# Performance work log

Measured on AMD Instinct MI355X. Metric: run time of the kernel, lower is better.

The kernel has to match this reference:

```python
import jax, jax.numpy as jnp
from jax import lax
import numpy as np

H = 64  # LSTM_HIDDEN_DIM
I = 3   # NUM_WEATHER_FEATURES


def _lstm_layer(x_seq, w_ih, w_hh, b_ih, b_hh):
    # x_seq: [B, T, in]; w_ih: [4H, in]; w_hh: [4H, H]; b_*: [4H]
    B = x_seq.shape[0]
    # Precompute input projections for all timesteps: [T, B, 4H]
    gx = jnp.einsum('bti,gi->tbg', x_seq, w_ih) + (b_ih + b_hh)
    h0 = jnp.zeros((B, H), dtype=x_seq.dtype)
    c0 = jnp.zeros((B, H), dtype=x_seq.dtype)

    def step(carry, g_t):
        h, c = carry
        gates = g_t + h @ w_hh.T  # [B, 4H]
        i, f, g, o = jnp.split(gates, 4, axis=-1)  # PyTorch gate order i,f,g,o
        i = jax.nn.sigmoid(i)
        f = jax.nn.sigmoid(f)
        g = jnp.tanh(g)
        o = jax.nn.sigmoid(o)
        c = f * c + i * g
        h = o * jnp.tanh(c)
        return (h, c), h

    (h_T, _), hs = lax.scan(step, (h0, c0), gx)
    # hs: [T, B, H] -> [B, T, H]
    return jnp.transpose(hs, (1, 0, 2)), h_T


def setup_inputs() -> dict:
    key = jax.random.key(0)
    ks = jax.random.split(key, 9)
    s = 1.0 / np.sqrt(H)  # PyTorch LSTM init scale
    x = jax.random.normal(ks[0], (4096, 365, I), dtype=jnp.float32)
    return {
        'x': x,
        'w_ih0': jax.random.uniform(ks[1], (4 * H, I), jnp.float32, -s, s),
        'w_hh0': jax.random.uniform(ks[2], (4 * H, H), jnp.float32, -s, s),
        'b_ih0': jax.random.uniform(ks[3], (4 * H,), jnp.float32, -s, s),
        'b_hh0': jax.random.uniform(ks[4], (4 * H,), jnp.float32, -s, s),
        'w_ih1': jax.random.uniform(ks[5], (4 * H, H), jnp.float32, -s, s),
        'w_hh1': jax.random.uniform(ks[6], (4 * H, H), jnp.float32, -s, s),
        'b_ih1': jax.random.uniform(ks[7], (4 * H,), jnp.float32, -s, s),
        'b_hh1': jax.random.uniform(ks[8], (4 * H,), jnp.float32, -s, s),
    }


def reference(x, w_ih0, w_hh0, b_ih0, b_hh0, w_ih1, w_hh1, b_ih1, b_hh1):
    # Layer 1 over raw features
    h1_seq, _ = _lstm_layer(x, w_ih0, w_hh0, b_ih0, b_hh0)
    # Layer 2 over layer-1 hidden states (eval mode: inter-layer dropout disabled)
    _, h2_T = _lstm_layer(h1_seq, w_ih1, w_hh1, b_ih1, b_hh1)
    # forward returns h_n[-1] == final hidden state of top layer: [B, H]
    return h2_T
```

## Files before the change

### kernel.cpp

```cpp
#include <hip/hip_runtime.h>

#define TT 365
#define NB 16
#define NTH 1024
#define XLEN (NB * TT * 3)

typedef _Float16 halfx8 __attribute__((ext_vector_type(8)));
typedef float floatx4 __attribute__((ext_vector_type(4)));
typedef float floatx2 __attribute__((ext_vector_type(2)));

#define MMH(A, B, C) __builtin_amdgcn_mfma_f32_16x16x32_f16((A), (B), (C), 0, 0, 0)

#define SGP -2.8853900817779268f
#define SGN  2.8853900817779268f
#define SS_  -1.4426950408889634f

static __device__ __forceinline__ float rcpf(float x) { return __builtin_amdgcn_rcpf(x); }
static __device__ __forceinline__ float ex2(float x)  { return __builtin_amdgcn_exp2f(x); }
static __device__ __forceinline__ unsigned short h16(float v) {
  _Float16 h = (_Float16)v;
  return __builtin_bit_cast(unsigned short, h);
}

#define LOADFRAG(SRC, SCALE, HI)                                               \
  do {                                                                         \
    _Pragma("unroll")                                                          \
    for (int jj = 0; jj < 8; ++jj) {                                           \
      (HI)[jj] = (_Float16)((SCALE) * (SRC)[jj]);                              \
    }                                                                          \
  } while (0)

#define PTAIL_CORE(PA, PB, CS2, HOUT)                                          \
  const floatx2 one_ = {1.0f, 1.0f};                                           \
  const floatx2 ei_ = {ex2((PA)[0]), ex2((PB)[0])};                            \
  const floatx2 ef_ = {ex2((PA)[1]), ex2((PB)[1])};                            \
  const floatx2 eg_ = {ex2((PA)[2]), ex2((PB)[2])};                            \
  const floatx2 eo_ = {ex2((PA)[3]), ex2((PB)[3])};                            \
  const floatx2 fd_ = one_ + ef_;                                              \
  const floatx2 fr_ = {rcpf(fd_.x), rcpf(fd_.y)};                              \
  const floatx2 P1_ = (one_ + ei_) * (one_ + eg_);                             \
  const floatx2 R1_ = {rcpf(P1_.x), rcpf(P1_.y)};                              \
  const floatx2 sgn2_ = {SGN, SGN};                                            \
  const floatx2 sgp2_ = {SGP, SGP};                                            \
  (CS2) = fr_ * (CS2) + (sgn2_ * eg_ + sgp2_) * R1_;                           \
  (CS2).x = fminf((CS2).x, 126.0f);                                            \
  (CS2).y = fminf((CS2).y, 126.0f);                                            \
  const floatx2 ec_ = {ex2((CS2).x), ex2((CS2).y)};                            \
  const floatx2 P2_ = (one_ + eo_) * (one_ + ec_);                             \
  const floatx2 R2_ = {rcpf(P2_.x), rcpf(P2_.y)};                              \
  const floatx2 HOUT = (one_ - ec_) * R2_;

#define PTAIL(PA, PB, CS2, ZW, IA, IB)                                         \
  do {                                                                         \
    PTAIL_CORE(PA, PB, CS2, hv_)                                               \
    (ZW)[IA] = h16(hv_.x);                                                     \
    (ZW)[IB] = h16(hv_.y);                                                     \
  } while (0)

__global__ __launch_bounds__(NTH)
__attribute__((amdgpu_waves_per_eu(4, 4)))
void lstm2_mfma10(
    const float* __restrict__ x,
    const float* __restrict__ w_ih0, const float* __restrict__ w_hh0,
    const float* __restrict__ b_ih0, const float* __restrict__ b_hh0,
    const float* __restrict__ w_ih1, const float* __restrict__ w_hh1,
    const float* __restrict__ b_ih1, const float* __restrict__ b_hh1,
    float* __restrict__ out)
{
  __shared__ __align__(16) unsigned short Z[2][2048];
  __shared__ __align__(16) float xlds[XLEN];

  const int tid  = threadIdx.x;
  const int lane = tid & 63;
  const int wv   = tid >> 6;
  const int n15  = lane & 15;
  const int quad = lane >> 4;
  const int bbase = blockIdx.x * NB;
  const float sA = ((n15 & 3) == 2) ? SGP : SS_;

  {
    const float* xg = x + (size_t)bbase * (TT * 3);
    for (int i = tid; i < XLEN; i += NTH) xlds[i] = xg[i];
    for (int i = tid; i < 2048; i += NTH) { Z[0][i] = 0; Z[1][i] = 0; }
  }
  unsigned short* const Zb0 = &Z[0][0];
  unsigned short* const Zb1 = &Z[1][0];
  __syncthreads();

  if (wv < 8) {
    const int w = wv;
    halfx8 a2[2][4];
    floatx4 b1v[2];
    #pragma unroll
    for (int tt = 0; tt < 2; ++tt) {
      const int mt   = 2 * w + tt;
      const int arow = (n15 & 3) * 64 + mt * 4 + (n15 >> 2);
      #pragma unroll
      for (int kt = 0; kt < 4; ++kt) {
        const int k0 = kt * 32 + quad * 8;
        const float* src = (k0 < 64) ? (w_ih1 + arow * 64 + k0)
                                     : (w_hh1 + arow * 64 + (k0 - 64));
        LOADFRAG(src, sA, a2[tt][kt]);
      }
      #pragma unroll
      for (int r = 0; r < 4; ++r) {
        const int crow = r * 64 + mt * 4 + quad;
        const float sC = (r == 2) ? SGP : SS_;
        b1v[tt][r] = sC * (b_ih1[crow] + b_hh1[crow]);
      }
    }
    const int j0 = 8 * w + quad, j1 = 8 * w + 4 + quad;
    const int si0 = 1024 + (j0 >> 5) * 512 + ((j0 >> 3) & 3) * 128 + n15 * 8 + (j0 & 7);
    const int si1 = 1024 + (j1 >> 5) * 512 + ((j1 >> 3) & 3) * 128 + n15 * 8 + (j1 & 7);
    floatx2 c2v = {0.f, 0.f};
    const halfx8* const Z0r = (const halfx8*)Zb0 + lane;
    const halfx8* const Z1r = (const halfx8*)Zb1 + lane;

    __syncthreads();

#define ESTEP(ZRP, ZW)                                                         \
    do {                                                                       \
      const halfx8 bh0 = (ZRP)[0],   bh1 = (ZRP)[64];                          \
      const halfx8 bh2 = (ZRP)[128], bh3 = (ZRP)[192];                         \
      floatx4 e0 = b1v[0], e1 = b1v[1];                                        \
      e0 = MMH(a2[0][0], bh0, e0); e0 = MMH(a2[0][1], bh1, e0);                \
      e0 = MMH(a2[0][2], bh2, e0); e0 = MMH(a2[0][3], bh3, e0);                \
      e1 = MMH(a2[1][0], bh0, e1); e1 = MMH(a2[1][1], bh1, e1);                \
      e1 = MMH(a2[1][2], bh2, e1); e1 = MMH(a2[1][3], bh3, e1);                \
      PTAIL(e0, e1, c2v, ZW, si0, si1);                                        \
      __syncthreads();                                                         \
    } while (0)

    for (int it = 0; it < 182; ++it) {
      ESTEP(Z0r, Zb1);
      ESTEP(Z1r, Zb0);
    }

    {
      const halfx8 bh0 = Z0r[0],   bh1 = Z0r[64];
      const halfx8 bh2 = Z0r[128], bh3 = Z0r[192];
      floatx4 e0 = b1v[0], e1 = b1v[1];
      e0 = MMH(a2[0][0], bh0, e0); e0 = MMH(a2[0][1], bh1, e0);
      e0 = MMH(a2[0][2], bh2, e0); e0 = MMH(a2[0][3], bh3, e0);
      e1 = MMH(a2[1][0], bh0, e1); e1 = MMH(a2[1][1], bh1, e1);
      e1 = MMH(a2[1][2], bh2, e1); e1 = MMH(a2[1][3], bh3, e1);
      PTAIL_CORE(e0, e1, c2v, hv_)
      out[(size_t)(bbase + n15) * 64 + j0] = hv_.x;
      out[(size_t)(bbase + n15) * 64 + j1] = hv_.y;
    }
  } else {
    const int u = wv - 8;
    halfx8 a1[2][2];
    floatx4 wiX[2], wiY[2], wiZ[2], b0v[2];
    #pragma unroll
    for (int tt = 0; tt < 2; ++tt) {
      const int mt   = 2 * u + tt;
      const int arow = (n15 & 3) * 64 + mt * 4 + (n15 >> 2);
      #pragma unroll
      for (int kt = 0; kt < 2; ++kt) {
        const float* src = w_hh0 + arow * 64 + kt * 32 + quad * 8;
        LOADFRAG(src, sA, a1[tt][kt]);
      }
      #pragma unroll
      for (int r = 0; r < 4; ++r) {
        const int crow = r * 64 + mt * 4 + quad;
        const float sC = (r == 2) ? SGP : SS_;
        wiX[tt][r] = sC * w_ih0[crow * 3 + 0];
        wiY[tt][r] = sC * w_ih0[crow * 3 + 1];
        wiZ[tt][r] = sC * w_ih0[crow * 3 + 2];
        b0v[tt][r] = sC * (b_ih0[crow] + b_hh0[crow]);
      }
    }
    const int j0 = 8 * u + quad, j1 = 8 * u + 4 + quad;
    const int si0 = (j0 >> 5) * 512 + ((j0 >> 3) & 3) * 128 + n15 * 8 + (j0 & 7);
    const int si1 = (j1 >> 5) * 512 + ((j1 >> 3) & 3) * 128 + n15 * 8 + (j1 & 7);
    floatx2 c1v = {0.f, 0.f};
    const halfx8* const Z0r = (const halfx8*)Zb0 + lane;
    const halfx8* const Z1r = (const halfx8*)Zb1 + lane;

    {
      const float xv0 = xlds[n15 * 1095 + 0];
      const float xv1 = xlds[n15 * 1095 + 1];
      const float xv2 = xlds[n15 * 1095 + 2];
      const floatx4 s0 = {xv0, xv0, xv0, xv0};
      const floatx4 s1 = {xv1, xv1, xv1, xv1};
      const floatx4 s2 = {xv2, xv2, xv2, xv2};
      floatx4 d0 = __builtin_elementwise_fma(wiX[0], s0,
                     __builtin_elementwise_fma(wiY[0], s1,
                       __builtin_elementwise_fma(wiZ[0], s2, b0v[0])));
      floatx4 d1 = __builtin_elementwise_fma(wiX[1], s0,
                     __builtin_elementwise_fma(wiY[1], s1,
                       __builtin_elementwise_fma(wiZ[1], s2, b0v[1])));
      PTAIL(d0, d1, c1v, Zb0, si0, si1);
    }
    __syncthreads();

    const float* xp = xlds + n15 * 1095 + 3;

#define DSTEP(ZRP, ZW)                                                         \
    do {                                                                       \
      const halfx8 bh0 = (ZRP)[0], bh1 = (ZRP)[64];                            \
      const float xv0 = xp[0], xv1 = xp[1], xv2 = xp[2];                       \
      const floatx4 s0 = {xv0, xv0, xv0, xv0};                                 \
      const floatx4 s1 = {xv1, xv1, xv1, xv1};                                 \
      const floatx4 s2 = {xv2, xv2, xv2, xv2};                                 \
      floatx4 d0 = __builtin_elementwise_fma(wiX[0], s0,                       \
                     __builtin_elementwise_fma(wiY[0], s1,                     \
                       __builtin_elementwise_fma(wiZ[0], s2, b0v[0])));        \
      floatx4 d1 = __builtin_elementwise_fma(wiX[1], s0,                       \
                     __builtin_elementwise_fma(wiY[1], s1,                     \
                       __builtin_elementwise_fma(wiZ[1], s2, b0v[1])));        \
      d0 = MMH(a1[0][0], bh0, d0); d0 = MMH(a1[0][1], bh1, d0);                \
      d1 = MMH(a1[1][0], bh0, d1); d1 = MMH(a1[1][1], bh1, d1);                \
      PTAIL(d0, d1, c1v, ZW, si0, si1);                                        \
      xp += 3;                                                                 \
      __syncthreads();                                                         \
    } while (0)

    for (int it = 0; it < 182; ++it) {
      DSTEP(Z0r, Zb1);
      DSTEP(Z1r, Zb0);
    }
  }
}

extern "C" void kernel_launch(void* const* d_in, const int* in_sizes, int n_in,
                              void* d_out, int out_size, void* d_ws, size_t ws_size,
                              hipStream_t stream) {
  const float* x     = (const float*)d_in[0];
  const float* w_ih0 = (const float*)d_in[1];
  const float* w_hh0 = (const float*)d_in[2];
  const float* b_ih0 = (const float*)d_in[3];
  const float* b_hh0 = (const float*)d_in[4];
  const float* w_ih1 = (const float*)d_in[5];
  const float* w_hh1 = (const float*)d_in[6];
  const float* b_ih1 = (const float*)d_in[7];
  const float* b_hh1 = (const float*)d_in[8];
  float* out = (float*)d_out;

  const int B = in_sizes[0] / (TT * 3);
  const int grid = B / NB;

  lstm2_mfma10<<<dim3(grid), dim3(NTH), 0, stream>>>(
      x, w_ih0, w_hh0, b_ih0, b_hh0, w_ih1, w_hh1, b_ih1, b_hh1, out);
}
```

Measured before the change: 311.9 us.

## Pack hidden-state writes, transpose x in LDS, merge cell-update reciprocals

Gate rows are remapped so each lane owns two adjacent hidden units. Their fp16 outputs can then be packed with cvt_pkrtz into one 32-bit LDS store per step instead of two 16-bit stores, and the final output is written as a float2. The input sequence is transposed in LDS to a [t][batch][4] layout so each step reads x with one 16-byte load. The cell update folds its two reciprocals into one with a common denominator, and the clamp is lowered to 60 to keep the larger product from overflowing. This shortens the per-step serial dependency chain. It risks precision loss from the product denominator and adds integer divides in the prologue.

```diff
diff --git a/kernel.cpp b/kernel.cpp
--- a/kernel.cpp
+++ b/kernel.cpp
@@ -17,10 +17,6 @@
 
 static __device__ __forceinline__ float rcpf(float x) { return __builtin_amdgcn_rcpf(x); }
 static __device__ __forceinline__ float ex2(float x)  { return __builtin_amdgcn_exp2f(x); }
-static __device__ __forceinline__ unsigned short h16(float v) {
-  _Float16 h = (_Float16)v;
-  return __builtin_bit_cast(unsigned short, h);
-}
 
 #define LOADFRAG(SRC, SCALE, HI)                                               \
   do {                                                                         \
@@ -36,30 +32,31 @@
   const floatx2 ef_ = {ex2((PA)[1]), ex2((PB)[1])};                            \
   const floatx2 eg_ = {ex2((PA)[2]), ex2((PB)[2])};                            \
   const floatx2 eo_ = {ex2((PA)[3]), ex2((PB)[3])};                            \
-  const floatx2 fd_ = one_ + ef_;                                              \
-  const floatx2 fr_ = {rcpf(fd_.x), rcpf(fd_.y)};                              \
-  const floatx2 P1_ = (one_ + ei_) * (one_ + eg_);                             \
-  const floatx2 R1_ = {rcpf(P1_.x), rcpf(P1_.y)};                              \
   const floatx2 sgn2_ = {SGN, SGN};                                            \
   const floatx2 sgp2_ = {SGP, SGP};                                            \
-  (CS2) = fr_ * (CS2) + (sgn2_ * eg_ + sgp2_) * R1_;                           \
-  (CS2).x = fminf((CS2).x, 126.0f);                                            \
-  (CS2).y = fminf((CS2).y, 126.0f);                                            \
+  const floatx2 fd_ = one_ + ef_;                                              \
+  const floatx2 P1_ = (one_ + ei_) * (one_ + eg_);                             \
+  const floatx2 Dp_ = P1_ * fd_;                                               \
+  const floatx2 R_  = {rcpf(Dp_.x), rcpf(Dp_.y)};                              \
+  const floatx2 T_  = (sgn2_ * eg_ + sgp2_) * fd_;                             \
+  (CS2) = ((CS2) * P1_ + T_) * R_;                                             \
+  (CS2).x = fminf((CS2).x, 60.0f);                                             \
+  (CS2).y = fminf((CS2).y, 60.0f);                                             \
   const floatx2 ec_ = {ex2((CS2).x), ex2((CS2).y)};                            \
   const floatx2 P2_ = (one_ + eo_) * (one_ + ec_);                             \
   const floatx2 R2_ = {rcpf(P2_.x), rcpf(P2_.y)};                              \
   const floatx2 HOUT = (one_ - ec_) * R2_;
 
-#define PTAIL(PA, PB, CS2, ZW, IA, IB)                                         \
+#define PTAIL(PA, PB, CS2, ZW32, WIDX)                                         \
   do {                                                                         \
     PTAIL_CORE(PA, PB, CS2, hv_)                                               \
-    (ZW)[IA] = h16(hv_.x);                                                     \
-    (ZW)[IB] = h16(hv_.y);                                                     \
+    (ZW32)[WIDX] =                                                             \
+        __builtin_bit_cast(unsigned, __builtin_amdgcn_cvt_pkrtz(hv_.x, hv_.y)); \
   } while (0)
 
 __global__ __launch_bounds__(NTH)
 __attribute__((amdgpu_waves_per_eu(4, 4)))
-void lstm2_mfma10(
+void lstm2_mfma11(
     const float* __restrict__ x,
     const float* __restrict__ w_ih0, const float* __restrict__ w_hh0,
     const float* __restrict__ b_ih0, const float* __restrict__ b_hh0,
@@ -68,7 +65,7 @@
     float* __restrict__ out)
 {
   __shared__ __align__(16) unsigned short Z[2][2048];
-  __shared__ __align__(16) float xlds[XLEN];
+  __shared__ __align__(16) float xh[TT * 16 * 4];
 
   const int tid  = threadIdx.x;
   const int lane = tid & 63;
@@ -80,12 +77,19 @@
 
   {
     const float* xg = x + (size_t)bbase * (TT * 3);
-    for (int i = tid; i < XLEN; i += NTH) xlds[i] = xg[i];
+    for (int i = tid; i < XLEN; i += NTH) {
+      const int b = i / 1095;
+      const int rem = i - b * 1095;
+      const int t = rem / 3;
+      const int c = rem - 3 * t;
+      xh[(t * 16 + b) * 4 + c] = xg[i];
+    }
     for (int i = tid; i < 2048; i += NTH) { Z[0][i] = 0; Z[1][i] = 0; }
   }
   unsigned short* const Zb0 = &Z[0][0];
   unsigned short* const Zb1 = &Z[1][0];
   __syncthreads();
+
 
   if (wv < 8) {
     const int w = wv;
@@ -93,8 +97,7 @@
     floatx4 b1v[2];
     #pragma unroll
     for (int tt = 0; tt < 2; ++tt) {
-      const int mt   = 2 * w + tt;
-      const int arow = (n15 & 3) * 64 + mt * 4 + (n15 >> 2);
+      const int arow = (n15 & 3) * 64 + 8 * w + 2 * (n15 >> 2) + tt;
       #pragma unroll
       for (int kt = 0; kt < 4; ++kt) {
         const int k0 = kt * 32 + quad * 8;
@@ -104,21 +107,20 @@
       }
       #pragma unroll
       for (int r = 0; r < 4; ++r) {
-        const int crow = r * 64 + mt * 4 + quad;
+        const int crow = r * 64 + 8 * w + 2 * quad + tt;
         const float sC = (r == 2) ? SGP : SS_;
         b1v[tt][r] = sC * (b_ih1[crow] + b_hh1[crow]);
       }
     }
-    const int j0 = 8 * w + quad, j1 = 8 * w + 4 + quad;
-    const int si0 = 1024 + (j0 >> 5) * 512 + ((j0 >> 3) & 3) * 128 + n15 * 8 + (j0 & 7);
-    const int si1 = 1024 + (j1 >> 5) * 512 + ((j1 >> 3) & 3) * 128 + n15 * 8 + (j1 & 7);
+    const int j0 = 8 * w + 2 * quad;
+    const int widx = 512 + (w >> 2) * 256 + (w & 3) * 64 + n15 * 4 + quad;
     floatx2 c2v = {0.f, 0.f};
     const halfx8* const Z0r = (const halfx8*)Zb0 + lane;
     const halfx8* const Z1r = (const halfx8*)Zb1 + lane;
 
     __syncthreads();
 
-#define ESTEP(ZRP, ZW)                                                         \
+#define ESTEP(ZRP, ZW32)                                                       \
     do {                                                                       \
       const halfx8 bh0 = (ZRP)[0],   bh1 = (ZRP)[64];                          \
       const halfx8 bh2 = (ZRP)[128], bh3 = (ZRP)[192];                         \
@@ -127,13 +129,13 @@
       e0 = MMH(a2[0][2], bh2, e0); e0 = MMH(a2[0][3], bh3, e0);                \
       e1 = MMH(a2[1][0], bh0, e1); e1 = MMH(a2[1][1], bh1, e1);                \
       e1 = MMH(a2[1][2], bh2, e1); e1 = MMH(a2[1][3], bh3, e1);                \
-      PTAIL(e0, e1, c2v, ZW, si0, si1);                                        \
+      PTAIL(e0, e1, c2v, ZW32, widx);                                          \
       __syncthreads();                                                         \
     } while (0)
 
     for (int it = 0; it < 182; ++it) {
-      ESTEP(Z0r, Zb1);
-      ESTEP(Z1r, Zb0);
+      ESTEP(Z0r, (unsigned*)Zb1);
+      ESTEP(Z1r, (unsigned*)Zb0);
     }
 
     {
@@ -145,8 +147,7 @@
       e1 = MMH(a2[1][0], bh0, e1); e1 = MMH(a2[1][1], bh1, e1);
       e1 = MMH(a2[1][2], bh2, e1); e1 = MMH(a2[1][3], bh3, e1);
       PTAIL_CORE(e0, e1, c2v, hv_)
-      out[(size_t)(bbase + n15) * 64 + j0] = hv_.x;
-      out[(size_t)(bbase + n15) * 64 + j1] = hv_.y;
+      *(floatx2*)(out + (size_t)(bbase + n15) * 64 + j0) = hv_;
     }
   } else {
     const int u = wv - 8;
@@ -154,8 +155,7 @@
     floatx4 wiX[2], wiY[2], wiZ[2], b0v[2];
     #pragma unroll
     for (int tt = 0; tt < 2; ++tt) {
-      const int mt   = 2 * u + tt;
-      const int arow = (n15 & 3) * 64 + mt * 4 + (n15 >> 2);
+      const int arow = (n15 & 3) * 64 + 8 * u + 2 * (n15 >> 2) + tt;
       #pragma unroll
       for (int kt = 0; kt < 2; ++kt) {
         const float* src = w_hh0 + arow * 64 + kt * 32 + quad * 8;
@@ -163,7 +163,7 @@
       }
       #pragma unroll
       for (int r = 0; r < 4; ++r) {
-        const int crow = r * 64 + mt * 4 + quad;
+        const int crow = r * 64 + 8 * u + 2 * quad + tt;
         const float sC = (r == 2) ? SGP : SS_;
         wiX[tt][r] = sC * w_ih0[crow * 3 + 0];
         wiY[tt][r] = sC * w_ih0[crow * 3 + 1];
@@ -171,39 +171,35 @@
         b0v[tt][r] = sC * (b_ih0[crow] + b_hh0[crow]);
       }
     }
-    const int j0 = 8 * u + quad, j1 = 8 * u + 4 + quad;
-    const int si0 = (j0 >> 5) * 512 + ((j0 >> 3) & 3) * 128 + n15 * 8 + (j0 & 7);
-    const int si1 = (j1 >> 5) * 512 + ((j1 >> 3) & 3) * 128 + n15 * 8 + (j1 & 7);
+    const int widx = (u >> 2) * 256 + (u & 3) * 64 + n15 * 4 + quad;
     floatx2 c1v = {0.f, 0.f};
     const halfx8* const Z0r = (const halfx8*)Zb0 + lane;
     const halfx8* const Z1r = (const halfx8*)Zb1 + lane;
 
     {
-      const float xv0 = xlds[n15 * 1095 + 0];
-      const float xv1 = xlds[n15 * 1095 + 1];
-      const float xv2 = xlds[n15 * 1095 + 2];
-      const floatx4 s0 = {xv0, xv0, xv0, xv0};
-      const floatx4 s1 = {xv1, xv1, xv1, xv1};
-      const floatx4 s2 = {xv2, xv2, xv2, xv2};
+      const floatx4 xv = *(const floatx4*)(xh + n15 * 4);
+      const floatx4 s0 = {xv[0], xv[0], xv[0], xv[0]};
+      const floatx4 s1 = {xv[1], xv[1], xv[1], xv[1]};
+      const floatx4 s2 = {xv[2], xv[2], xv[2], xv[2]};
       floatx4 d0 = __builtin_elementwise_fma(wiX[0], s0,
                      __builtin_elementwise_fma(wiY[0], s1,
                        __builtin_elementwise_fma(wiZ[0], s2, b0v[0])));
       floatx4 d1 = __builtin_elementwise_fma(wiX[1], s0,
                      __builtin_elementwise_fma(wiY[1], s1,
                        __builtin_elementwise_fma(wiZ[1], s2, b0v[1])));
-      PTAIL(d0, d1, c1v, Zb0, si0, si1);
+      PTAIL(d0, d1, c1v, (unsigned*)Zb0, widx);
     }
     __syncthreads();
 
-    const float* xp = xlds + n15 * 1095 + 3;
-
-#define DSTEP(ZRP, ZW)                                                         \
+    const float* xp = xh + 64 + n15 * 4;
+
+#define DSTEP(ZRP, ZW32)                                                       \
     do {                                                                       \
       const halfx8 bh0 = (ZRP)[0], bh1 = (ZRP)[64];                            \
-      const float xv0 = xp[0], xv1 = xp[1], xv2 = xp[2];                       \
-      const floatx4 s0 = {xv0, xv0, xv0, xv0};                                 \
-      const floatx4 s1 = {xv1, xv1, xv1, xv1};                                 \
-      const floatx4 s2 = {xv2, xv2, xv2, xv2};                                 \
+      const floatx4 xv = *(const floatx4*)xp;                                  \
+      const floatx4 s0 = {xv[0], xv[0], xv[0], xv[0]};                         \
+      const floatx4 s1 = {xv[1], xv[1], xv[1], xv[1]};                         \
+      const floatx4 s2 = {xv[2], xv[2], xv[2], xv[2]};                         \
       floatx4 d0 = __builtin_elementwise_fma(wiX[0], s0,                       \
                      __builtin_elementwise_fma(wiY[0], s1,                     \
                        __builtin_elementwise_fma(wiZ[0], s2, b0v[0])));        \
@@ -212,14 +208,14 @@
                        __builtin_elementwise_fma(wiZ[1], s2, b0v[1])));        \
       d0 = MMH(a1[0][0], bh0, d0); d0 = MMH(a1[0][1], bh1, d0);                \
       d1 = MMH(a1[1][0], bh0, d1); d1 = MMH(a1[1][1], bh1, d1);                \
-      PTAIL(d0, d1, c1v, ZW, si0, si1);                                        \
-      xp += 3;                                                                 \
+      PTAIL(d0, d1, c1v, ZW32, widx);                                          \
+      xp += 64;                                                                \
       __syncthreads();                                                         \
     } while (0)
 
     for (int it = 0; it < 182; ++it) {
-      DSTEP(Z0r, Zb1);
-      DSTEP(Z1r, Zb0);
+      DSTEP(Z0r, (unsigned*)Zb1);
+      DSTEP(Z1r, (unsigned*)Zb0);
     }
   }
 }
@@ -241,6 +237,6 @@
   const int B = in_sizes[0] / (TT * 3);
   const int grid = B / NB;
 
-  lstm2_mfma10<<<dim3(grid), dim3(NTH), 0, stream>>>(
+  lstm2_mfma11<<<dim3(grid), dim3(NTH), 0, stream>>>(
       x, w_ih0, w_hh0, b_ih0, b_hh0, w_ih1, w_hh1, b_ih1, b_hh1, out);
 }
```

Result: faster. 304.8 us (-2.3%).
